# Optimization experiments

Hardware: AMD Instinct MI355X
Metric: run time of the kernel (lower is better)

## Reference

```python
import jax, jax.numpy as jnp
import numpy as np
import math

B, T, C = 2, 2048, 1024
N_HEAD = 16
HEAD_DIM = C // N_HEAD


def setup_inputs() -> dict:
    key = jax.random.key(0)
    k1, k2, k3 = jax.random.split(key, 3)
    x = jax.random.normal(k1, (B, T, C), dtype=jnp.float32)
    # causal mask: positions where mask == 0 get -inf
    mask = jnp.tril(jnp.ones((T, T), dtype=bool))[None, None, :, :]
    W_attn = jax.random.normal(k2, (C, 3 * C), dtype=jnp.float32) * (1.0 / math.sqrt(C))
    b_attn = jnp.zeros((3 * C,), dtype=jnp.float32)
    W_proj = jax.random.normal(k3, (C, C), dtype=jnp.float32) * (1.0 / math.sqrt(C))
    b_proj = jnp.zeros((C,), dtype=jnp.float32)
    return {"x": x, "mask": mask, "W_attn": W_attn, "b_attn": b_attn,
            "W_proj": W_proj, "b_proj": b_proj}


def reference(x, mask, W_attn, b_attn, W_proj, b_proj):
    Bx, Tx, Cx = x.shape
    qkv = x @ W_attn + b_attn                      # [B,T,3C]
    q, k, v = jnp.split(qkv, 3, axis=2)
    # [B,T,C] -> [B,H,T,D]
    q = q.reshape(Bx, Tx, N_HEAD, HEAD_DIM).transpose(0, 2, 1, 3)
    k = k.reshape(Bx, Tx, N_HEAD, HEAD_DIM).transpose(0, 2, 1, 3)
    v = v.reshape(Bx, Tx, N_HEAD, HEAD_DIM).transpose(0, 2, 1, 3)
    scale = 1.0 / math.sqrt(HEAD_DIM)
    att = jnp.einsum('bhqd,bhkd->bhqk', q, k) * scale   # [B,H,T,T]
    att = jnp.where(mask, att, -jnp.inf)
    att = jax.nn.softmax(att, axis=-1)
    y = jnp.einsum('bhqk,bhkd->bhqd', att, v)            # [B,H,T,D]
    y = y.transpose(0, 2, 1, 3).reshape(Bx, Tx, Cx)      # [B,T,C]
    return y @ W_proj + b_proj
```

## Files before the change

### kernel.cpp

```cpp
#include <hip/hip_runtime.h>
#include <hip/hip_bf16.h>
#include <cstdint>

typedef unsigned short u16;
typedef unsigned int u32;
typedef unsigned long long u64;
using f32x4 = __attribute__((ext_vector_type(4))) float;
using s16x8 = __attribute__((ext_vector_type(8))) short;
using u32x4 = __attribute__((ext_vector_type(4))) u32;

#define NB 2
#define NT 2048
#define NC 1024
#define NH 16
#define HD 64

__device__ __forceinline__ u16 f2b(float f) {
    unsigned u = __float_as_uint(f);
    unsigned r = (u + 0x7FFFu + ((u >> 16) & 1u)) >> 16;
    return (u16)r;
}

__device__ __forceinline__ u32 cvtpk(float a, float b) {
    u32 r;
    asm("v_cvt_pk_bf16_f32 %0, %1, %2" : "=v"(r) : "v"(a), "v"(b));
    return r;
}
__device__ __forceinline__ void swap32(u32& a, u32& b) {
    asm("v_permlane32_swap_b32 %0, %1" : "+v"(a), "+v"(b));
}
__device__ __forceinline__ void swap16(u32& a, u32& b) {
    asm("v_permlane16_swap_b32 %0, %1" : "+v"(a), "+v"(b));
}

__device__ __forceinline__ void gl_lds16(const void* g, const void* l) {
    __builtin_amdgcn_global_load_lds(
        (const __attribute__((address_space(1))) unsigned int*)g,
        (__attribute__((address_space(3))) unsigned int*)l, 16, 0, 0);
}

__global__ __launch_bounds__(256) void conv_bf16(const float* __restrict__ in,
                                                 u16* __restrict__ out, int n4) {
    int i = blockIdx.x * 256 + threadIdx.x;
    if (i >= n4) return;
    float4 v = ((const float4*)in)[i];
    u64 pack = (u64)f2b(v.x) | ((u64)f2b(v.y) << 16) |
               ((u64)f2b(v.z) << 32) | ((u64)f2b(v.w) << 48);
    ((u64*)out)[i] = pack;
}

__global__ __launch_bounds__(256) void transpose_bf16(const float* __restrict__ W,
                                                      u16* __restrict__ Wt,
                                                      int K, int N) {
    __shared__ u16 s[64][65];
    const int n0 = blockIdx.x * 64, k0 = blockIdx.y * 64;
    const int t = threadIdx.x;
    const int tr = t >> 4, tc4 = (t & 15) * 4;
#pragma unroll
    for (int i = 0; i < 4; i++) {
        int r = tr + i * 16;
        float4 v = *(const float4*)&W[(size_t)(k0 + r) * N + n0 + tc4];
        s[r][tc4 + 0] = f2b(v.x);
        s[r][tc4 + 1] = f2b(v.y);
        s[r][tc4 + 2] = f2b(v.z);
        s[r][tc4 + 3] = f2b(v.w);
    }
    __syncthreads();
#pragma unroll
    for (int i = 0; i < 4; i++) {
        int nl = tr + i * 16;
        u64 pack = (u64)s[tc4 + 0][nl] | ((u64)s[tc4 + 1][nl] << 16) |
                   ((u64)s[tc4 + 2][nl] << 32) | ((u64)s[tc4 + 3][nl] << 48);
        *(u64*)&Wt[(size_t)(n0 + nl) * K + k0 + tc4] = pack;
    }
}

template <int OUT_BF16>
__global__ __launch_bounds__(256) void gemm_bt(const u16* __restrict__ A,
                                               const u16* __restrict__ Bt,
                                               const float* __restrict__ bias,
                                               void* __restrict__ Cout,
                                               int M, int N, int K) {
    __shared__ u16 As[128 * 32];
    __shared__ u16 Bs[128 * 32];
    const int tid = threadIdx.x;
    const int lane = tid & 63, w = tid >> 6;
    const int m0 = blockIdx.y * 128, n0 = blockIdx.x * 128;
    const int wm = w >> 1, wn = w & 1;
    f32x4 acc[4][4] = {};

    const int srow = 32 * w + (lane >> 2);
    const int scol = (lane & 3) * 8;

    for (int k0 = 0; k0 < K; k0 += 32) {
        gl_lds16(&A[(size_t)(m0 + srow) * K + k0 + scol], &As[w * 1024 + lane * 8]);
        gl_lds16(&A[(size_t)(m0 + srow + 16) * K + k0 + scol], &As[w * 1024 + 512 + lane * 8]);
        gl_lds16(&Bt[(size_t)(n0 + srow) * K + k0 + scol], &Bs[w * 1024 + lane * 8]);
        gl_lds16(&Bt[(size_t)(n0 + srow + 16) * K + k0 + scol], &Bs[w * 1024 + 512 + lane * 8]);
        __syncthreads();

        s16x8 af[4], bf[4];
#pragma unroll
        for (int mt = 0; mt < 4; mt++)
            af[mt] = *(const s16x8*)&As[(wm * 64 + mt * 16 + (lane & 15)) * 32 + (lane >> 4) * 8];
#pragma unroll
        for (int nt = 0; nt < 4; nt++)
            bf[nt] = *(const s16x8*)&Bs[(wn * 64 + nt * 16 + (lane & 15)) * 32 + (lane >> 4) * 8];
#pragma unroll
        for (int mt = 0; mt < 4; mt++)
#pragma unroll
            for (int nt = 0; nt < 4; nt++)
                acc[mt][nt] = __builtin_amdgcn_mfma_f32_16x16x32_bf16(af[mt], bf[nt], acc[mt][nt], 0, 0, 0);
        __syncthreads();
    }

#pragma unroll
    for (int mt = 0; mt < 4; mt++) {
        int row = m0 + wm * 64 + mt * 16 + (lane >> 4) * 4;
#pragma unroll
        for (int nt = 0; nt < 4; nt++) {
            int col = n0 + wn * 64 + nt * 16 + (lane & 15);
            float bs = bias[col];
#pragma unroll
            for (int r = 0; r < 4; r++) {
                float v = acc[mt][nt][r] + bs;
                if (OUT_BF16)
                    ((u16*)Cout)[(size_t)(row + r) * N + col] = f2b(v);
                else
                    ((float*)Cout)[(size_t)(row + r) * N + col] = v;
            }
        }
    }
}

__global__ __launch_bounds__(256) void gemm_bt_n64(const u16* __restrict__ A,
                                                   const u16* __restrict__ Bt,
                                                   const float* __restrict__ bias,
                                                   float* __restrict__ Cout,
                                                   int M, int N, int K) {
    __shared__ u16 As[128 * 32];
    __shared__ u16 Bs[64 * 32];
    const int tid = threadIdx.x;
    const int lane = tid & 63, w = tid >> 6;
    const int m0 = blockIdx.y * 128, n0 = blockIdx.x * 64;
    f32x4 acc[2][4] = {};

    const int srow = 32 * w + (lane >> 2);
    const int srowB = 16 * w + (lane >> 2);
    const int scol = (lane & 3) * 8;

    for (int k0 = 0; k0 < K; k0 += 32) {
        gl_lds16(&A[(size_t)(m0 + srow) * K + k0 + scol], &As[w * 1024 + lane * 8]);
        gl_lds16(&A[(size_t)(m0 + srow + 16) * K + k0 + scol], &As[w * 1024 + 512 + lane * 8]);
        gl_lds16(&Bt[(size_t)(n0 + srowB) * K + k0 + scol], &Bs[w * 512 + lane * 8]);
        __syncthreads();

        s16x8 af[2], bf[4];
#pragma unroll
        for (int mt = 0; mt < 2; mt++)
            af[mt] = *(const s16x8*)&As[(w * 32 + mt * 16 + (lane & 15)) * 32 + (lane >> 4) * 8];
#pragma unroll
        for (int nt = 0; nt < 4; nt++)
            bf[nt] = *(const s16x8*)&Bs[(nt * 16 + (lane & 15)) * 32 + (lane >> 4) * 8];
#pragma unroll
        for (int mt = 0; mt < 2; mt++)
#pragma unroll
            for (int nt = 0; nt < 4; nt++)
                acc[mt][nt] = __builtin_amdgcn_mfma_f32_16x16x32_bf16(af[mt], bf[nt], acc[mt][nt], 0, 0, 0);
        __syncthreads();
    }

#pragma unroll
    for (int mt = 0; mt < 2; mt++) {
        int row = m0 + w * 32 + mt * 16 + (lane >> 4) * 4;
#pragma unroll
        for (int nt = 0; nt < 4; nt++) {
            int col = n0 + nt * 16 + (lane & 15);
            float bs = bias[col];
#pragma unroll
            for (int r = 0; r < 4; r++)
                Cout[(size_t)(row + r) * N + col] = acc[mt][nt][r] + bs;
        }
    }
}

__global__ __launch_bounds__(256) void v_transpose(const u16* __restrict__ qkv,
                                                   u16* __restrict__ Vt) {
    __shared__ __align__(16) u16 s[64][72];
    const int t0 = blockIdx.x * 64;
    const int b = blockIdx.y >> 4, h = blockIdx.y & 15;
    const int t = threadIdx.x;
    const int r = t >> 2, c0 = (t & 3) * 16;
    const u16* src = qkv + (size_t)b * NT * (3 * NC) + (size_t)(t0 + r) * (3 * NC) + 2 * NC + h * HD + c0;
    *(s16x8*)&s[r][c0] = *(const s16x8*)src;
    *(s16x8*)&s[r][c0 + 8] = *(const s16x8*)(src + 8);
    __syncthreads();
    u32 arr[8];
#pragma unroll
    for (int jj = 0; jj < 8; jj++)
        arr[jj] = (u32)s[c0 + 2 * jj][r] | ((u32)s[c0 + 2 * jj + 1][r] << 16);
    u16* dst = Vt + ((size_t)(b * NH + h) * HD + r) * NT + t0 + c0;
    u32x4 lo, hi;
    lo[0] = arr[0]; lo[1] = arr[1]; lo[2] = arr[2]; lo[3] = arr[3];
    hi[0] = arr[4]; hi[1] = arr[5]; hi[2] = arr[6]; hi[3] = arr[7];
    *(u32x4*)dst = lo;
    *(u32x4*)(dst + 8) = hi;
}

__global__ __launch_bounds__(512) void attn_kernel(const u16* __restrict__ qkv,
                                                   const u16* __restrict__ Vt,
                                                   u16* __restrict__ yb) {
    __shared__ __align__(16) u16 Kb[2][2][64 * 64];
    __shared__ __align__(16) u16 Vb[2][2][64 * 64];

    const int l = threadIdx.x & 63;
    const int q16 = l & 15, g = l >> 4;
    const int wv = threadIdx.x >> 6;
    const int rg = wv & 3, hf = wv >> 2;
    const int i0 = blockIdx.x;
    const int xcd = i0 & 7, idx = i0 >> 3;
    const int hh = xcd * 4 + (idx >> 4);
    const int pr = idx & 15;
    const int b = hh >> 4, h = hh & 15;

    const u16* qkvb = qkv + (size_t)b * NT * (3 * NC);

    const int srow = l >> 3;
    const int sc8 = (l & 7) ^ (srow & 7);
    const u16* kSrc0 = qkvb + NC + h * HD + (size_t)(8 * rg + srow) * (3 * NC) + sc8 * 8;
    const u16* kSrc1 = kSrc0 + (size_t)32 * (3 * NC);
    const u16* vSrc0 = Vt + ((size_t)(b * NH + h) * HD + 8 * rg + srow) * NT + sc8 * 8;
    const u16* vSrc1 = vSrc0 + (size_t)32 * NT;

    const float sc2 = 0.125f * 1.44269504088896340736f;
    const float SHIFT = 5.0f * 1.44269504088896340736f;
    const int sw = q16 & 7;

    auto STAGE = [&](int t) {
        const int buf = t & 1;
        const size_t kOff = (size_t)t * 64 * (3 * NC);
        const int vOff = t * 64;
        gl_lds16(kSrc0 + kOff, &Kb[hf][buf][rg * 512 + l * 8]);
        gl_lds16(kSrc1 + kOff, &Kb[hf][buf][2048 + rg * 512 + l * 8]);
        gl_lds16(vSrc0 + vOff, &Vb[hf][buf][rg * 512 + l * 8]);
        gl_lds16(vSrc1 + vOff, &Vb[hf][buf][2048 + rg * 512 + l * 8]);
    };

#pragma unroll 1
    for (int sc = 0; sc < 2; ++sc) {
        const int cc = (sc == 0) ? (31 - pr) : pr;
        const int nt = cc + 1;
        const int h0 = (nt + 1) >> 1;
        const int base = hf ? h0 : 0;
        const int myN = hf ? (nt - h0) : h0;
        const int qw = cc * 64 + 16 * rg;

        s16x8 qf[2];
#pragma unroll
        for (int kc = 0; kc < 2; kc++)
            qf[kc] = *(const s16x8*)(qkvb + (size_t)(qw + q16) * (3 * NC) + h * HD + kc * 32 + g * 8);

        f32x4 yacc[4] = {};
        float lsum = 0.f;

        if (myN > 0) STAGE(base);
        for (int u = 0; u < h0; ++u) {
            const int t = base + u;
            const bool act = (u < myN);
            if (act && (u + 1 < myN)) {
                STAGE(t + 1);
                asm volatile("s_waitcnt vmcnt(4)" ::: "memory");
            } else {
                asm volatile("s_waitcnt vmcnt(0)" ::: "memory");
            }
            __builtin_amdgcn_s_barrier();

            if (act) {
                const u16* Kc = &Kb[hf][t & 1][0];
                const u16* Vc = &Vb[hf][t & 1][0];

                s16x8 kf[4][2];
#pragma unroll
                for (int ii = 0; ii < 4; ii++)
#pragma unroll
                    for (int kc = 0; kc < 2; kc++)
                        kf[ii][kc] = *(const s16x8*)&Kc[(16 * ii + q16) * 64 + ((4 * kc + g) ^ sw) * 8];

                s16x8 vf0[4];
#pragma unroll
                for (int dt = 0; dt < 4; dt++)
                    vf0[dt] = *(const s16x8*)&Vc[(16 * dt + q16) * 64 + (g ^ sw) * 8];

                f32x4 sacc[4] = {};
                __builtin_amdgcn_s_setprio(1);
#pragma unroll
                for (int ii = 0; ii < 4; ii++)
#pragma unroll
                    for (int kc = 0; kc < 2; kc++)
                        sacc[ii] = __builtin_amdgcn_mfma_f32_16x16x32_bf16(kf[ii][kc], qf[kc], sacc[ii], 0, 0, 0);
                __builtin_amdgcn_s_setprio(0);

                if (t == cc) {
                    const int kv0 = t * 64;
#pragma unroll
                    for (int ii = 0; ii < 4; ii++)
#pragma unroll
                        for (int r = 0; r < 4; r++)
                            if (kv0 + 16 * ii + 4 * g + r > qw + q16) sacc[ii][r] = -1e30f;
                }

                float p[4][4];
                float ps = 0.f;
#pragma unroll
                for (int ii = 0; ii < 4; ii++)
#pragma unroll
                    for (int r = 0; r < 4; r++) {
                        p[ii][r] = exp2f(fmaf(sacc[ii][r], sc2, -SHIFT));
                        ps += p[ii][r];
                    }
                lsum += ps;

                s16x8 pfrag[2];
#pragma unroll
                for (int ks = 0; ks < 2; ks++) {
                    u32 C0 = cvtpk(p[2 * ks][0], p[2 * ks][1]);
                    u32 C1 = cvtpk(p[2 * ks][2], p[2 * ks][3]);
                    u32 D0 = cvtpk(p[2 * ks + 1][0], p[2 * ks + 1][1]);
                    u32 D1 = cvtpk(p[2 * ks + 1][2], p[2 * ks + 1][3]);
                    swap32(C0, D0); swap16(C0, D0);
                    swap32(C1, D1); swap16(C1, D1);
                    u32x4 fr;
                    fr[0] = C0; fr[1] = C1; fr[2] = D0; fr[3] = D1;
                    pfrag[ks] = __builtin_bit_cast(s16x8, fr);
                }

                s16x8 vf1[4];
#pragma unroll
                for (int dt = 0; dt < 4; dt++)
                    vf1[dt] = *(const s16x8*)&Vc[(16 * dt + q16) * 64 + ((4 + g) ^ sw) * 8];

                __builtin_amdgcn_s_setprio(1);
#pragma unroll
                for (int dt = 0; dt < 4; dt++)
                    yacc[dt] = __builtin_amdgcn_mfma_f32_16x16x32_bf16(vf0[dt], pfrag[0], yacc[dt], 0, 0, 0);
#pragma unroll
                for (int dt = 0; dt < 4; dt++)
                    yacc[dt] = __builtin_amdgcn_mfma_f32_16x16x32_bf16(vf1[dt], pfrag[1], yacc[dt], 0, 0, 0);
                __builtin_amdgcn_s_setprio(0);
            }

            __builtin_amdgcn_s_barrier();
        }

        float* mY = (float*)&Kb[1][0][0];
        float* mL = (float*)&Vb[1][0][0];
        if (hf == 1) {
#pragma unroll
            for (int dt = 0; dt < 4; dt++)
#pragma unroll
                for (int r = 0; r < 4; r++)
                    mY[(rg * 16 + dt * 4 + r) * 64 + l] = yacc[dt][r];
            mL[rg * 64 + l] = lsum;
        }
        __syncthreads();
        if (hf == 0) {
#pragma unroll
            for (int dt = 0; dt < 4; dt++)
#pragma unroll
                for (int r = 0; r < 4; r++)
                    yacc[dt][r] += mY[(rg * 16 + dt * 4 + r) * 64 + l];
            lsum += mL[rg * 64 + l];
            lsum += __shfl_xor(lsum, 16);
            lsum += __shfl_xor(lsum, 32);
            float inv = 1.f / lsum;
            size_t rowoff = ((size_t)(b * NT + qw + q16)) * NC + h * HD;
#pragma unroll
            for (int dt = 0; dt < 4; dt++) {
                u32 lo = cvtpk(yacc[dt][0] * inv, yacc[dt][1] * inv);
                u32 hi = cvtpk(yacc[dt][2] * inv, yacc[dt][3] * inv);
                u64 pk = (u64)lo | ((u64)hi << 32);
                *(u64*)(yb + rowoff + 16 * dt + 4 * g) = pk;
            }
        }
        __syncthreads();
    }
}

extern "C" void kernel_launch(void* const* d_in, const int* in_sizes, int n_in,
                              void* d_out, int out_size, void* d_ws, size_t ws_size,
                              hipStream_t stream) {
    const float* x  = (const float*)d_in[0];
    const float* Wa = (const float*)d_in[2];
    const float* ba = (const float*)d_in[3];
    const float* Wp = (const float*)d_in[4];
    const float* bp = (const float*)d_in[5];
    float* out = (float*)d_out;

    char* ws = (char*)d_ws;
    u16* xb  = (u16*)(ws);
    u16* WaT = (u16*)(ws + (8ull << 20));
    u16* WpT = (u16*)(ws + (14ull << 20));
    u16* qkv = (u16*)(ws + (16ull << 20));
    u16* yb  = (u16*)(ws + (40ull << 20));
    u16* Vtb = (u16*)(ws + (48ull << 20));

    const int M = NB * NT;

    conv_bf16<<<(M * NC / 4 + 255) / 256, 256, 0, stream>>>(x, xb, M * NC / 4);
    transpose_bf16<<<dim3(3 * NC / 64, NC / 64), 256, 0, stream>>>(Wa, WaT, NC, 3 * NC);
    transpose_bf16<<<dim3(NC / 64, NC / 64), 256, 0, stream>>>(Wp, WpT, NC, NC);

    gemm_bt<1><<<dim3(3 * NC / 128, M / 128), 256, 0, stream>>>(xb, WaT, ba, qkv, M, 3 * NC, NC);

    v_transpose<<<dim3(NT / 64, NB * NH), 256, 0, stream>>>(qkv, Vtb);

    attn_kernel<<<dim3(NB * NH * 16), 512, 0, stream>>>(qkv, Vtb, yb);

    gemm_bt_n64<<<dim3(NC / 64, M / 128), 256, 0, stream>>>(yb, WpT, bp, out, M, NC, NC);
}
```

Before: 122.2 us.

## Rework V transpose access pattern and precompute attention LDS/global addresses

The V transpose kernel now uses a padded 64x65 shared tile with 8-byte loads and stores instead of 16-byte vectors, with the aim of cutting LDS bank conflicts on the column reads. In the attention kernel, the per-lane swizzled LDS fragment offsets are computed once before the loop. Global staging pointers are now advanced incrementally rather than recomputed from the tile index each step, to reduce integer address arithmetic in the hot loop. The narrower global accesses in the transpose may lower memory efficiency there.

```diff
diff --git a/kernel.cpp b/kernel.cpp
--- a/kernel.cpp
+++ b/kernel.cpp
@@ -186,25 +186,30 @@
 
 __global__ __launch_bounds__(256) void v_transpose(const u16* __restrict__ qkv,
                                                    u16* __restrict__ Vt) {
-    __shared__ __align__(16) u16 s[64][72];
+    __shared__ u16 s[64][65];
     const int t0 = blockIdx.x * 64;
     const int b = blockIdx.y >> 4, h = blockIdx.y & 15;
     const int t = threadIdx.x;
-    const int r = t >> 2, c0 = (t & 3) * 16;
-    const u16* src = qkv + (size_t)b * NT * (3 * NC) + (size_t)(t0 + r) * (3 * NC) + 2 * NC + h * HD + c0;
-    *(s16x8*)&s[r][c0] = *(const s16x8*)src;
-    *(s16x8*)&s[r][c0 + 8] = *(const s16x8*)(src + 8);
+    const int tr = t >> 4, tc4 = (t & 15) * 4;
+    const u16* src = qkv + (size_t)b * NT * (3 * NC) + 2 * NC + h * HD;
+#pragma unroll
+    for (int i = 0; i < 4; i++) {
+        int r = tr + i * 16;
+        u64 v = *(const u64*)&src[(size_t)(t0 + r) * (3 * NC) + tc4];
+        s[r][tc4 + 0] = (u16)v;
+        s[r][tc4 + 1] = (u16)(v >> 16);
+        s[r][tc4 + 2] = (u16)(v >> 32);
+        s[r][tc4 + 3] = (u16)(v >> 48);
+    }
     __syncthreads();
-    u32 arr[8];
-#pragma unroll
-    for (int jj = 0; jj < 8; jj++)
-        arr[jj] = (u32)s[c0 + 2 * jj][r] | ((u32)s[c0 + 2 * jj + 1][r] << 16);
-    u16* dst = Vt + ((size_t)(b * NH + h) * HD + r) * NT + t0 + c0;
-    u32x4 lo, hi;
-    lo[0] = arr[0]; lo[1] = arr[1]; lo[2] = arr[2]; lo[3] = arr[3];
-    hi[0] = arr[4]; hi[1] = arr[5]; hi[2] = arr[6]; hi[3] = arr[7];
-    *(u32x4*)dst = lo;
-    *(u32x4*)(dst + 8) = hi;
+    u16* dstb = Vt + (size_t)(b * NH + h) * HD * NT;
+#pragma unroll
+    for (int i = 0; i < 4; i++) {
+        int d = tr + i * 16;
+        u64 pack = (u64)s[tc4 + 0][d] | ((u64)s[tc4 + 1][d] << 16) |
+                   ((u64)s[tc4 + 2][d] << 32) | ((u64)s[tc4 + 3][d] << 48);
+        *(u64*)&dstb[(size_t)d * NT + t0 + tc4] = pack;
+    }
 }
 
 __global__ __launch_bounds__(512) void attn_kernel(const u16* __restrict__ qkv,
@@ -231,20 +236,23 @@
     const u16* kSrc1 = kSrc0 + (size_t)32 * (3 * NC);
     const u16* vSrc0 = Vt + ((size_t)(b * NH + h) * HD + 8 * rg + srow) * NT + sc8 * 8;
     const u16* vSrc1 = vSrc0 + (size_t)32 * NT;
+    const size_t kStep = (size_t)64 * (3 * NC);
 
     const float sc2 = 0.125f * 1.44269504088896340736f;
     const float SHIFT = 5.0f * 1.44269504088896340736f;
     const int sw = q16 & 7;
 
-    auto STAGE = [&](int t) {
-        const int buf = t & 1;
-        const size_t kOff = (size_t)t * 64 * (3 * NC);
-        const int vOff = t * 64;
-        gl_lds16(kSrc0 + kOff, &Kb[hf][buf][rg * 512 + l * 8]);
-        gl_lds16(kSrc1 + kOff, &Kb[hf][buf][2048 + rg * 512 + l * 8]);
-        gl_lds16(vSrc0 + vOff, &Vb[hf][buf][rg * 512 + l * 8]);
-        gl_lds16(vSrc1 + vOff, &Vb[hf][buf][2048 + rg * 512 + l * 8]);
-    };
+    u32 kfo[4][2], vfo[2][4];
+#pragma unroll
+    for (int ii = 0; ii < 4; ii++)
+#pragma unroll
+        for (int kc = 0; kc < 2; kc++)
+            kfo[ii][kc] = (u32)(((16 * ii + q16) * 64 + ((4 * kc + g) ^ sw) * 8) * 2);
+#pragma unroll
+    for (int ks = 0; ks < 2; ks++)
+#pragma unroll
+        for (int dt = 0; dt < 4; dt++)
+            vfo[ks][dt] = (u32)(((16 * dt + q16) * 64 + ((4 * ks + g) ^ sw) * 8) * 2);
 
 #pragma unroll 1
     for (int sc = 0; sc < 2; ++sc) {
@@ -263,12 +271,25 @@
         f32x4 yacc[4] = {};
         float lsum = 0.f;
 
-        if (myN > 0) STAGE(base);
+        const u16* kP0 = kSrc0 + (size_t)base * kStep;
+        const u16* kP1 = kSrc1 + (size_t)base * kStep;
+        const u16* vP0 = vSrc0 + base * 64;
+        const u16* vP1 = vSrc1 + base * 64;
+
+        auto STAGE = [&](int buf) {
+            gl_lds16(kP0, &Kb[hf][buf][rg * 512 + l * 8]);
+            gl_lds16(kP1, &Kb[hf][buf][2048 + rg * 512 + l * 8]);
+            gl_lds16(vP0, &Vb[hf][buf][rg * 512 + l * 8]);
+            gl_lds16(vP1, &Vb[hf][buf][2048 + rg * 512 + l * 8]);
+            kP0 += kStep; kP1 += kStep; vP0 += 64; vP1 += 64;
+        };
+
+        if (myN > 0) STAGE(base & 1);
         for (int u = 0; u < h0; ++u) {
             const int t = base + u;
             const bool act = (u < myN);
             if (act && (u + 1 < myN)) {
-                STAGE(t + 1);
+                STAGE((t + 1) & 1);
                 asm volatile("s_waitcnt vmcnt(4)" ::: "memory");
             } else {
                 asm volatile("s_waitcnt vmcnt(0)" ::: "memory");
@@ -276,20 +297,20 @@
             __builtin_amdgcn_s_barrier();
 
             if (act) {
-                const u16* Kc = &Kb[hf][t & 1][0];
-                const u16* Vc = &Vb[hf][t & 1][0];
+                const char* Kc = (const char*)&Kb[hf][t & 1][0];
+                const char* Vc = (const char*)&Vb[hf][t & 1][0];
 
                 s16x8 kf[4][2];
 #pragma unroll
                 for (int ii = 0; ii < 4; ii++)
 #pragma unroll
                     for (int kc = 0; kc < 2; kc++)
-                        kf[ii][kc] = *(const s16x8*)&Kc[(16 * ii + q16) * 64 + ((4 * kc + g) ^ sw) * 8];
+                        kf[ii][kc] = *(const s16x8*)(Kc + kfo[ii][kc]);
 
                 s16x8 vf0[4];
 #pragma unroll
                 for (int dt = 0; dt < 4; dt++)
-                    vf0[dt] = *(const s16x8*)&Vc[(16 * dt + q16) * 64 + (g ^ sw) * 8];
+                    vf0[dt] = *(const s16x8*)(Vc + vfo[0][dt]);
 
                 f32x4 sacc[4] = {};
                 __builtin_amdgcn_s_setprio(1);
@@ -337,7 +358,7 @@
                 s16x8 vf1[4];
 #pragma unroll
                 for (int dt = 0; dt < 4; dt++)
-                    vf1[dt] = *(const s16x8*)&Vc[(16 * dt + q16) * 64 + ((4 + g) ^ sw) * 8];
+                    vf1[dt] = *(const s16x8*)(Vc + vfo[1][dt]);
 
                 __builtin_amdgcn_s_setprio(1);
 #pragma unroll
```

New measurement: 122.5 us. Within noise of the previous version (+0.2%).
